# Optimization experiments

Hardware: AMD Instinct MI355X
Metric: run time of the kernel (lower is better)

The kernel has to match this reference:

```python
import jax, jax.numpy as jnp
import numpy as np

B, T, N = 8, 20, 256
BN = B * N
IN_DIM, H, HEADS, DH = 2, 128, 8, 16
FF = 4 * H
LAYERS = 5
EPS = 1e-5


def _ln(h, g, b):
    mu = h.mean(-1, keepdims=True)
    v = ((h - mu) ** 2).mean(-1, keepdims=True)
    return (h - mu) * jax.lax.rsqrt(v + EPS) * g + b


def setup_inputs() -> dict:
    key = jax.random.key(0)
    ks = jax.random.split(key, 16)
    ego_mask = jax.random.uniform(ks[0], (B, T, N)) > 0.2
    ego_mask = ego_mask.at[:, 0, :].set(True)  # every node active at t=0 (no fully-padded sequence)
    x_raw = jax.random.normal(ks[1], (T, BN, IN_DIM), dtype=jnp.float32)
    adj = (jax.random.uniform(ks[2], (T, BN, BN)) < 0.01).astype(jnp.float32)
    s = 0.02
    p = {}
    p['gcn1_w'] = jax.random.normal(ks[3], (IN_DIM, H), jnp.float32) * s
    p['gcn_ws'] = jax.random.normal(ks[4], (5, H, H), jnp.float32) * s
    p['gcn_bs'] = jnp.zeros((6, H), jnp.float32)
    p['ln_g'] = jnp.ones((6, H), jnp.float32)
    p['ln_b'] = jnp.zeros((6, H), jnp.float32)
    p['pos_embed'] = jax.random.normal(ks[5], (T, H), jnp.float32) * s
    p['t_wqkv'] = jax.random.normal(ks[6], (LAYERS, 3 * H, H), jnp.float32) * s
    p['t_bqkv'] = jnp.zeros((LAYERS, 3 * H), jnp.float32)
    p['t_wo'] = jax.random.normal(ks[7], (LAYERS, H, H), jnp.float32) * s
    p['t_bo'] = jnp.zeros((LAYERS, H), jnp.float32)
    p['t_ln1g'] = jnp.ones((LAYERS, H), jnp.float32)
    p['t_ln1b'] = jnp.zeros((LAYERS, H), jnp.float32)
    p['t_w1'] = jax.random.normal(ks[8], (LAYERS, FF, H), jnp.float32) * s
    p['t_b1'] = jnp.zeros((LAYERS, FF), jnp.float32)
    p['t_w2'] = jax.random.normal(ks[9], (LAYERS, H, FF), jnp.float32) * s
    p['t_b2'] = jnp.zeros((LAYERS, H), jnp.float32)
    p['t_ln2g'] = jnp.ones((LAYERS, H), jnp.float32)
    p['t_ln2b'] = jnp.zeros((LAYERS, H), jnp.float32)
    return dict(ego_mask=ego_mask, x_raw=x_raw, adj=adj, **p)


def _forward(ego_mask, x_raw, adj, gcn1_w, gcn_ws, gcn_bs, ln_g, ln_b, pos_embed,
             t_wqkv, t_bqkv, t_wo, t_bo, t_ln1g, t_ln1b, t_w1, t_b1, t_w2, t_b2,
             t_ln2g, t_ln2b):
    mask_flat = ego_mask.transpose(1, 0, 2).reshape(T, BN).astype(x_raw.dtype)  # [T, BN]

    def per_t(x_t, A_t, m):
        # masked subgraph + self-loops only on active nodes (PyG GCNConv on x[idx], A[idx][:,idx])
        Am = A_t * m[:, None] * m[None, :]
        Ahat = Am + jnp.diag(m)
        deg = Ahat.sum(0)                       # gcn_norm: degree at target (col of edge_index)
        dinv = jnp.where(deg > 0, jax.lax.rsqrt(deg), 0.0)
        S = (dinv[:, None] * Ahat * dinv[None, :]).T  # out[dst] = sum_src norm * x[src]

        def gcn(h, W, b):
            return S @ (h @ W) + b

        h = jax.nn.relu(_ln(gcn(x_t, gcn1_w, gcn_bs[0]), ln_g[0], ln_b[0]))
        for i in range(5):
            hr = _ln(gcn(h, gcn_ws[i], gcn_bs[i + 1]), ln_g[i + 1], ln_b[i + 1])
            h = jax.nn.relu(hr + h)  # residual then ReLU, as in source
        return h * m[:, None]        # inactive rows stay zero (x_placeholder)

    x_ph = jax.vmap(per_t)(x_raw, adj, mask_flat)          # [T, BN, H]
    x = x_ph.transpose(1, 0, 2) + pos_embed[None]          # [BN, T, H]

    # src_key_padding_mask: True = padded -> -inf on keys
    key_bias = jnp.where(mask_flat.T.astype(bool), 0.0, -jnp.inf)[:, None, None, :]  # [BN,1,1,T]
    scale = 1.0 / np.sqrt(DH)
    for l in range(LAYERS):  # post-norm TransformerEncoderLayer, activation=relu, eval (no dropout)
        qkv = x @ t_wqkv[l].T + t_bqkv[l]
        q, k, v = jnp.split(qkv, 3, axis=-1)
        q = q.reshape(BN, T, HEADS, DH)
        k = k.reshape(BN, T, HEADS, DH)
        v = v.reshape(BN, T, HEADS, DH)
        sc = jnp.einsum('bqhd,bkhd->bhqk', q, k) * scale + key_bias
        a = jax.nn.softmax(sc, axis=-1)
        o = jnp.einsum('bhqk,bkhd->bqhd', a, v).reshape(BN, T, H)
        o = o @ t_wo[l].T + t_bo[l]
        x = _ln(x + o, t_ln1g[l], t_ln1b[l])
        ff = jax.nn.relu(x @ t_w1[l].T + t_b1[l]) @ t_w2[l].T + t_b2[l]
        x = _ln(x + ff, t_ln2g[l], t_ln2b[l])
    return x.reshape(B, N, T, H)


def reference(ego_mask, x_raw, adj, gcn1_w, gcn_ws, gcn_bs, ln_g, ln_b, pos_embed,
              t_wqkv, t_bqkv, t_wo, t_bo, t_ln1g, t_ln1b, t_w1, t_b1, t_w2, t_b2,
              t_ln2g, t_ln2b):
    return _forward(ego_mask, x_raw, adj, gcn1_w, gcn_ws, gcn_bs, ln_g, ln_b,
                    pos_embed, t_wqkv, t_bqkv, t_wo, t_bo, t_ln1g, t_ln1b,
                    t_w1, t_b1, t_w2, t_b2, t_ln2g, t_ln2b)
```

## Files before the change

kernel.cpp:

```cpp
#include <hip/hip_runtime.h>
#include <hip/hip_bf16.h>
#include <cstdint>
#include <cstddef>

#define BNODES 2048
#define NT 20
#define HDIM 128
#define NROWS (NT * BNODES)
#define CAP 64
#define QP 129

typedef __attribute__((ext_vector_type(8))) short short8;
typedef __attribute__((ext_vector_type(4))) float floatx4;

__device__ __forceinline__ float bf2f(short u) {
  return __uint_as_float(((unsigned int)(unsigned short)u) << 16);
}

__global__ void setup_kernel(const void* __restrict__ ego, float* __restrict__ maskf,
                             int* __restrict__ colcnt,
                             const float* __restrict__ twqkv, const float* __restrict__ two,
                             const float* __restrict__ tw1, const float* __restrict__ tw2,
                             const float* __restrict__ gcnws,
                             __hip_bfloat16* __restrict__ wqkv, __hip_bfloat16* __restrict__ wo,
                             __hip_bfloat16* __restrict__ w1, __hip_bfloat16* __restrict__ w2,
                             __hip_bfloat16* __restrict__ wsT) {
  int gid = blockIdx.x * blockDim.x + threadIdx.x;
  if (gid < NROWS) {
    unsigned int w0 = ((const unsigned int*)ego)[0];
    int val;
    if (w0 == 1u)                 val = ((const int*)ego)[gid] != 0;
    else if (w0 == 0x3F800000u)   val = ((const float*)ego)[gid] != 0.0f;
    else if (w0 == 0x3F803F80u)   val = ((const unsigned short*)ego)[gid] != 0;
    else                          val = ((const unsigned char*)ego)[gid] != 0;
    int b = gid / (NT * 256);
    int t = (gid / 256) % NT;
    int n = gid % 256;
    maskf[t * BNODES + b * 256 + n] = val ? 1.0f : 0.0f;
    colcnt[gid] = 0;
    return;
  }
  gid -= NROWS;
  if (gid < 245760) { wqkv[gid] = __float2bfloat16(twqkv[gid]); return; }
  gid -= 245760;
  if (gid < 81920) { wo[gid] = __float2bfloat16(two[gid]); return; }
  gid -= 81920;
  if (gid < 327680) { w1[gid] = __float2bfloat16(tw1[gid]); return; }
  gid -= 327680;
  if (gid < 327680) { w2[gid] = __float2bfloat16(tw2[gid]); return; }
  gid -= 327680;
  if (gid < 81920) {
    int l = gid >> 14, rem = gid & 16383;
    int n = rem >> 7, k = rem & 127;
    wsT[gid] = __float2bfloat16(gcnws[(l << 14) + (k << 7) + n]);
  }
}

__global__ __launch_bounds__(256) void build_edges_kernel(const float* __restrict__ adj,
                                                          const float* __restrict__ maskf,
                                                          int* __restrict__ colcnt,
                                                          int* __restrict__ colidx) {
  size_t e4 = (size_t)blockIdx.x * 256 + threadIdx.x;
  size_t e = e4 * 4;
  size_t row = e >> 11;
  if (maskf[row] == 0.0f) return;
  const float4 a = ((const float4*)adj)[e4];
  if (a.x == 0.0f && a.y == 0.0f && a.z == 0.0f && a.w == 0.0f) return;
  int i0 = (int)(e & (BNODES - 1));
  int t = (int)(row >> 11);
  int j = (int)(row & (BNODES - 1));
  int base = t * BNODES;
  if (a.x != 0.0f) { int p = atomicAdd(&colcnt[base + i0 + 0], 1); if (p < CAP) colidx[(size_t)(base + i0 + 0) * CAP + p] = j; }
  if (a.y != 0.0f) { int p = atomicAdd(&colcnt[base + i0 + 1], 1); if (p < CAP) colidx[(size_t)(base + i0 + 1) * CAP + p] = j; }
  if (a.z != 0.0f) { int p = atomicAdd(&colcnt[base + i0 + 2], 1); if (p < CAP) colidx[(size_t)(base + i0 + 2) * CAP + p] = j; }
  if (a.w != 0.0f) { int p = atomicAdd(&colcnt[base + i0 + 3], 1); if (p < CAP) colidx[(size_t)(base + i0 + 3) * CAP + p] = j; }
}

__global__ void finalize_deg_kernel(const float* __restrict__ maskf, int* __restrict__ colcnt,
                                    float* __restrict__ dinv) {
  int gid = blockIdx.x * blockDim.x + threadIdx.x;
  if (gid >= NROWS) return;
  int cnt = colcnt[gid];
  dinv[gid] = (maskf[gid] != 0.0f) ? rsqrtf((float)cnt + 1.0f) : 0.0f;
  colcnt[gid] = cnt < CAP ? cnt : CAP;
}

__global__ __launch_bounds__(HDIM) void spmm_ln0_kernel(const float* __restrict__ xraw,
                                                        const float* __restrict__ gw,
                                                        const float* __restrict__ dinv,
                                                        const int* __restrict__ colcnt,
                                                        const int* __restrict__ colidx,
                                                        const float* __restrict__ bias,
                                                        const float* __restrict__ gamma,
                                                        const float* __restrict__ beta,
                                                        float* __restrict__ dstF,
                                                        __hip_bfloat16* __restrict__ dstB) {
  int r = blockIdx.x, c = threadIdx.x;
  int t = r >> 11;
  float di = dinv[r];
  float g0 = gw[c], g1 = gw[HDIM + c];
  float acc = 0.0f;
  if (di != 0.0f) {
    acc = di * fmaf(xraw[2 * r], g0, xraw[2 * r + 1] * g1);
    int cnt = colcnt[r];
    const int* cols = colidx + (size_t)r * CAP;
    const float* dt = dinv + t * BNODES;
    for (int k = 0; k < cnt; ++k) {
      int j = cols[k];
      size_t gr = (size_t)t * BNODES + j;
      acc = fmaf(dt[j], fmaf(xraw[2 * gr], g0, xraw[2 * gr + 1] * g1), acc);
    }
    acc *= di;
  }
  float v = acc + bias[c];
  float s = v, q = v * v;
  #pragma unroll
  for (int off = 32; off > 0; off >>= 1) {
    s += __shfl_down(s, off, 64);
    q += __shfl_down(q, off, 64);
  }
  __shared__ float ls[2], lq2[2];
  int wid = c >> 6, lane = c & 63;
  if (lane == 0) { ls[wid] = s; lq2[wid] = q; }
  __syncthreads();
  float mu = (ls[0] + ls[1]) * (1.0f / HDIM);
  float var = fmaxf((lq2[0] + lq2[1]) * (1.0f / HDIM) - mu * mu, 0.0f);
  float rs = rsqrtf(var + 1e-5f);
  float o = fmaxf((v - mu) * rs * gamma[c] + beta[c], 0.0f);
  size_t oi = (size_t)r * HDIM + c;
  dstF[oi] = o;
  dstB[oi] = __float2bfloat16(o);
}

__global__ __launch_bounds__(HDIM) void spmm_kernel(const __hip_bfloat16* __restrict__ Y,
                                                    const float* __restrict__ dinv,
                                                    const int* __restrict__ colcnt,
                                                    const int* __restrict__ colidx,
                                                    __hip_bfloat16* __restrict__ out) {
  int r = blockIdx.x, c = threadIdx.x;
  int t = r >> 11;
  float di = dinv[r];
  size_t oi = (size_t)r * HDIM + c;
  if (di == 0.0f) { out[oi] = __float2bfloat16(0.0f); return; }
  const short* Ys = (const short*)Y;
  float acc = di * bf2f(Ys[oi]);
  int cnt = colcnt[r];
  const int* cols = colidx + (size_t)r * CAP;
  const float* dt = dinv + t * BNODES;
  const short* Yt = Ys + (size_t)t * BNODES * HDIM;
  for (int k = 0; k < cnt; ++k) {
    int j = cols[k];
    acc = fmaf(dt[j], bf2f(Yt[(size_t)j * HDIM + c]), acc);
  }
  out[oi] = __float2bfloat16(di * acc);
}

__device__ __forceinline__ void async16(const void* g, void* l) {
  __builtin_amdgcn_global_load_lds(
      (const __attribute__((address_space(1))) unsigned int*)g,
      (__attribute__((address_space(3))) unsigned int*)l, 16, 0, 0);
}

__global__ __launch_bounds__(256) void gemm_plain(const __hip_bfloat16* __restrict__ A,
                                                  const __hip_bfloat16* __restrict__ Bt,
                                                  const float* __restrict__ bias,
                                                  int K, int N, int relu,
                                                  __hip_bfloat16* __restrict__ Cb) {
  __shared__ __align__(16) char smem[65536];
  __hip_bfloat16* As = (__hip_bfloat16*)smem;
  __hip_bfloat16* Bs = As + 128 * 128;
  const int tid = threadIdx.x;
  const int wv = tid >> 6, ln = tid & 63;
  const int n0 = blockIdx.x << 7, m0 = blockIdx.y << 7;
  const int wm = (wv & 1) << 6, wn = (wv >> 1) << 6;
  const int lr = ln & 15, lq = ln >> 4;

  floatx4 acc[4][4];
  #pragma unroll
  for (int mi = 0; mi < 4; ++mi)
    #pragma unroll
    for (int ni = 0; ni < 4; ++ni) acc[mi][ni] = (floatx4)0.0f;

  for (int k0 = 0; k0 < K; k0 += 128) {
    if (k0) __syncthreads();
    #pragma unroll
    for (int i = 0; i < 8; ++i) {
      int rloc = i * 16 + wv * 4 + lq;
      int sc = (ln & 15) ^ (rloc & 15);
      async16((const char*)A + ((size_t)(m0 + rloc) * K + k0) * 2 + (size_t)sc * 16,
              (char*)As + (size_t)(i * 16 + wv * 4) * 256);
      async16((const char*)Bt + ((size_t)(n0 + rloc) * K + k0) * 2 + (size_t)sc * 16,
              (char*)Bs + (size_t)(i * 16 + wv * 4) * 256);
    }
    __syncthreads();
    #pragma unroll
    for (int kc = 0; kc < 4; ++kc) {
      short8 af[4], bfr[4];
      #pragma unroll
      for (int mi = 0; mi < 4; ++mi) {
        int R = wm + (mi << 4) + lr;
        int ch = ((kc << 2) + lq) ^ (R & 15);
        af[mi] = *(const short8*)(As + (R << 7) + (ch << 3));
      }
      #pragma unroll
      for (int ni = 0; ni < 4; ++ni) {
        int R = wn + (ni << 4) + lr;
        int ch = ((kc << 2) + lq) ^ (R & 15);
        bfr[ni] = *(const short8*)(Bs + (R << 7) + (ch << 3));
      }
      #pragma unroll
      for (int mi = 0; mi < 4; ++mi)
        #pragma unroll
        for (int ni = 0; ni < 4; ++ni)
          acc[mi][ni] = __builtin_amdgcn_mfma_f32_16x16x32_bf16(af[mi], bfr[ni], acc[mi][ni], 0, 0, 0);
    }
  }
  #pragma unroll
  for (int ni = 0; ni < 4; ++ni) {
    int cn = n0 + wn + (ni << 4) + lr;
    float bv = bias ? bias[cn] : 0.0f;
    #pragma unroll
    for (int mi = 0; mi < 4; ++mi) {
      #pragma unroll
      for (int r = 0; r < 4; ++r) {
        int rm = m0 + wm + (mi << 4) + (lq << 2) + r;
        float v = acc[mi][ni][r] + bv;
        if (relu) v = fmaxf(v, 0.0f);
        Cb[(size_t)rm * N + cn] = __float2bfloat16(v);
      }
    }
  }
}

__global__ __launch_bounds__(256) void gemm_ln(const __hip_bfloat16* __restrict__ A,
                                               const __hip_bfloat16* __restrict__ Bt,
                                               const float* __restrict__ bias,
                                               int K, int gcn_mode,
                                               const float* __restrict__ residF,
                                               const float* __restrict__ lng,
                                               const float* __restrict__ lnb,
                                               const float* __restrict__ maskf,
                                               const float* __restrict__ pos,
                                               float* __restrict__ outF,
                                               __hip_bfloat16* __restrict__ outB) {
  __shared__ __align__(16) char smem[49152];
  __hip_bfloat16* As = (__hip_bfloat16*)smem;
  __hip_bfloat16* Bs = As + 64 * 128;
  float* Cs = (float*)smem;
  const int tid = threadIdx.x;
  const int wv = tid >> 6, ln = tid & 63;
  const int m0 = blockIdx.x << 6;
  const int wm = (wv & 1) << 5, wn = (wv >> 1) << 6;
  const int lr = ln & 15, lq = ln >> 4;

  floatx4 acc[2][4];
  #pragma unroll
  for (int mi = 0; mi < 2; ++mi)
    #pragma unroll
    for (int ni = 0; ni < 4; ++ni) acc[mi][ni] = (floatx4)0.0f;

  for (int k0 = 0; k0 < K; k0 += 128) {
    if (k0) __syncthreads();
    #pragma unroll
    for (int i = 0; i < 4; ++i) {
      int rloc = i * 16 + wv * 4 + lq;
      int sc = (ln & 15) ^ (rloc & 15);
      async16((const char*)A + ((size_t)(m0 + rloc) * K + k0) * 2 + (size_t)sc * 16,
              (char*)As + (size_t)(i * 16 + wv * 4) * 256);
    }
    #pragma unroll
    for (int i = 0; i < 8; ++i) {
      int rloc = i * 16 + wv * 4 + lq;
      int sc = (ln & 15) ^ (rloc & 15);
      async16((const char*)Bt + ((size_t)rloc * K + k0) * 2 + (size_t)sc * 16,
              (char*)Bs + (size_t)(i * 16 + wv * 4) * 256);
    }
    __syncthreads();
    #pragma unroll
    for (int kc = 0; kc < 4; ++kc) {
      short8 af[2], bfr[4];
      #pragma unroll
      for (int mi = 0; mi < 2; ++mi) {
        int R = wm + (mi << 4) + lr;
        int ch = ((kc << 2) + lq) ^ (R & 15);
        af[mi] = *(const short8*)(As + (R << 7) + (ch << 3));
      }
      #pragma unroll
      for (int ni = 0; ni < 4; ++ni) {
        int R = wn + (ni << 4) + lr;
        int ch = ((kc << 2) + lq) ^ (R & 15);
        bfr[ni] = *(const short8*)(Bs + (R << 7) + (ch << 3));
      }
      #pragma unroll
      for (int mi = 0; mi < 2; ++mi)
        #pragma unroll
        for (int ni = 0; ni < 4; ++ni)
          acc[mi][ni] = __builtin_amdgcn_mfma_f32_16x16x32_bf16(af[mi], bfr[ni], acc[mi][ni], 0, 0, 0);
    }
  }

  __syncthreads();
  #pragma unroll
  for (int ni = 0; ni < 4; ++ni) {
    int cn = wn + (ni << 4) + lr;
    float bv = bias[cn];
    #pragma unroll
    for (int mi = 0; mi < 2; ++mi) {
      #pragma unroll
      for (int r = 0; r < 4; ++r) {
        int rl = wm + (mi << 4) + (lq << 2) + r;
        float v = acc[mi][ni][r] + bv;
        if (!gcn_mode) v += residF[(size_t)(m0 + rl) * HDIM + cn];
        Cs[(rl << 7) + cn] = v;
      }
    }
  }
  __syncthreads();
  float2 gam = *(const float2*)(lng + ln * 2);
  float2 bet = *(const float2*)(lnb + ln * 2);
  #pragma unroll 4
  for (int p = 0; p < 16; ++p) {
    int rl = p * 4 + wv;
    int grow = m0 + rl;
    float2 xv = *(const float2*)(Cs + (rl << 7) + ln * 2);
    float s = xv.x + xv.y, q = xv.x * xv.x + xv.y * xv.y;
    #pragma unroll
    for (int off = 32; off > 0; off >>= 1) {
      s += __shfl_xor(s, off, 64);
      q += __shfl_xor(q, off, 64);
    }
    float mu = s * (1.0f / HDIM);
    float var = fmaxf(q * (1.0f / HDIM) - mu * mu, 0.0f);
    float rs = rsqrtf(var + 1e-5f);
    float o0 = (xv.x - mu) * rs * gam.x + bet.x;
    float o1 = (xv.y - mu) * rs * gam.y + bet.y;
    if (gcn_mode) {
      float2 rv = *(const float2*)(residF + (size_t)grow * HDIM + ln * 2);
      o0 = fmaxf(o0 + rv.x, 0.0f);
      o1 = fmaxf(o1 + rv.y, 0.0f);
    }
    size_t oi;
    if (pos) {
      int t = grow >> 11, bn = grow & (BNODES - 1);
      float m = maskf[grow];
      float2 pv = *(const float2*)(pos + t * HDIM + ln * 2);
      o0 = o0 * m + pv.x;
      o1 = o1 * m + pv.y;
      oi = ((size_t)bn * NT + t) * HDIM + ln * 2;
    } else {
      oi = (size_t)grow * HDIM + ln * 2;
    }
    if (outF) *(float2*)(outF + oi) = make_float2(o0, o1);
    if (outB) {
      __hip_bfloat16 b0 = __float2bfloat16(o0), b1 = __float2bfloat16(o1);
      unsigned int pk = ((unsigned int)*(unsigned short*)&b1 << 16) | *(unsigned short*)&b0;
      *(unsigned int*)((char*)outB + oi * 2) = pk;
    }
  }
}

__global__ __launch_bounds__(256) void attn_kernel(const __hip_bfloat16* __restrict__ qkv,
                                                   const float* __restrict__ maskf,
                                                   __hip_bfloat16* __restrict__ o) {
  int bn = blockIdx.x;
  __shared__ float q[NT][QP], kk[NT][QP], vv[NT][QP];
  __shared__ float sc[8][NT][NT];
  __shared__ float mb[NT];
  int tid = threadIdx.x;
  if (tid < NT) mb[tid] = (maskf[tid * BNODES + bn] == 0.0f) ? -1e30f : 0.0f;
  for (int idx = tid; idx < NT * 48; idx += 256) {
    int t = idx / 48, c8 = idx % 48;
    short8 v8 = *(const short8*)((const short*)qkv + ((size_t)bn * NT + t) * 384 + c8 * 8);
    float* dst = (c8 < 16) ? &q[t][c8 * 8] : (c8 < 32) ? &kk[t][(c8 - 16) * 8] : &vv[t][(c8 - 32) * 8];
    #pragma unroll
    for (int i = 0; i < 8; ++i) dst[i] = bf2f(v8[i]);
  }
  __syncthreads();
  for (int idx = tid; idx < 8 * NT * NT; idx += 256) {
    int h = idx / (NT * NT), rr = idx % (NT * NT);
    int tq = rr / NT, tk = rr % NT;
    float s = 0.0f;
    #pragma unroll
    for (int d = 0; d < 16; ++d) s += q[tq][h * 16 + d] * kk[tk][h * 16 + d];
    sc[h][tq][tk] = s * 0.25f + mb[tk];
  }
  __syncthreads();
  if (tid < 8 * NT) {
    int h = tid / NT, tq = tid % NT;
    float mx = -1e30f;
    for (int tk = 0; tk < NT; ++tk) mx = fmaxf(mx, sc[h][tq][tk]);
    float sum = 0.0f;
    for (int tk = 0; tk < NT; ++tk) { float e = __expf(sc[h][tq][tk] - mx); sc[h][tq][tk] = e; sum += e; }
    float inv = 1.0f / sum;
    for (int tk = 0; tk < NT; ++tk) sc[h][tq][tk] *= inv;
  }
  __syncthreads();
  for (int idx = tid; idx < NT * HDIM; idx += 256) {
    int tq = idx / HDIM, col = idx % HDIM;
    int h = col >> 4;
    float s = 0.0f;
    #pragma unroll
    for (int tk = 0; tk < NT; ++tk) s += sc[h][tq][tk] * vv[tk][col];
    o[((size_t)bn * NT + tq) * HDIM + col] = __float2bfloat16(s);
  }
}

extern "C" void kernel_launch(void* const* d_in, const int* in_sizes, int n_in,
                              void* d_out, int out_size, void* d_ws, size_t ws_size,
                              hipStream_t stream) {
  const void*  ego   = d_in[0];
  const float* xraw  = (const float*)d_in[1];
  const float* adj   = (const float*)d_in[2];
  const float* gcn1w = (const float*)d_in[3];
  const float* gcnws = (const float*)d_in[4];
  const float* gcnbs = (const float*)d_in[5];
  const float* lng   = (const float*)d_in[6];
  const float* lnb   = (const float*)d_in[7];
  const float* pos   = (const float*)d_in[8];
  const float* twqkv = (const float*)d_in[9];
  const float* tbqkv = (const float*)d_in[10];
  const float* two   = (const float*)d_in[11];
  const float* tbo   = (const float*)d_in[12];
  const float* tln1g = (const float*)d_in[13];
  const float* tln1b = (const float*)d_in[14];
  const float* tw1   = (const float*)d_in[15];
  const float* tb1   = (const float*)d_in[16];
  const float* tw2   = (const float*)d_in[17];
  const float* tb2   = (const float*)d_in[18];
  const float* tln2g = (const float*)d_in[19];
  const float* tln2b = (const float*)d_in[20];

  char* base = (char*)d_ws;
  size_t off = 0;
  auto alloc = [&](size_t bytes) -> void* {
    void* p = base + off;
    off = (off + bytes + 255) & ~(size_t)255;
    return p;
  };
  float* maskf  = (float*)alloc((size_t)NROWS * 4);
  float* dinv   = (float*)alloc((size_t)NROWS * 4);
  int*   colcnt = (int*)  alloc((size_t)NROWS * 4);
  void*  regA   = alloc((size_t)NROWS * 384 * 2);
  int*   colidx = (int*)regA;
  __hip_bfloat16* qkv_bf = (__hip_bfloat16*)regA;
  void*  regB   = alloc((size_t)NROWS * 512 * 2);
  __hip_bfloat16* g_bf   = (__hip_bfloat16*)regB;
  __hip_bfloat16* big_bf = (__hip_bfloat16*)regB;
  __hip_bfloat16* attn_bf = (__hip_bfloat16*)alloc((size_t)NROWS * HDIM * 2);
  __hip_bfloat16* hbufA   = (__hip_bfloat16*)alloc((size_t)NROWS * HDIM * 2);
  __hip_bfloat16* xbf     = (__hip_bfloat16*)alloc((size_t)NROWS * HDIM * 2);
  float* hbufF  = (float*)alloc((size_t)NROWS * HDIM * 4);
  float* xbuf   = (float*)alloc((size_t)NROWS * HDIM * 4);
  __hip_bfloat16* wqkv_bf = (__hip_bfloat16*)alloc((size_t)245760 * 2);
  __hip_bfloat16* wo_bf   = (__hip_bfloat16*)alloc((size_t)81920 * 2);
  __hip_bfloat16* w1_bf   = (__hip_bfloat16*)alloc((size_t)327680 * 2);
  __hip_bfloat16* w2_bf   = (__hip_bfloat16*)alloc((size_t)327680 * 2);
  __hip_bfloat16* wsT_bf  = (__hip_bfloat16*)alloc((size_t)81920 * 2);

  setup_kernel<<<4320, 256, 0, stream>>>(ego, maskf, colcnt, twqkv, two, tw1, tw2, gcnws,
                                         wqkv_bf, wo_bf, w1_bf, w2_bf, wsT_bf);
  build_edges_kernel<<<81920, 256, 0, stream>>>(adj, maskf, colcnt, colidx);
  finalize_deg_kernel<<<160, 256, 0, stream>>>(maskf, colcnt, dinv);

  spmm_ln0_kernel<<<NROWS, HDIM, 0, stream>>>(xraw, gcn1w, dinv, colcnt, colidx,
                                              gcnbs, lng, lnb, hbufF, hbufA);
  for (int i = 0; i < 5; ++i) {
    spmm_kernel<<<NROWS, HDIM, 0, stream>>>(hbufA, dinv, colcnt, colidx, g_bf);
    const float* fm = (i == 4) ? maskf : nullptr;
    const float* fp = (i == 4) ? pos : nullptr;
    float* oF = (i == 4) ? xbuf : hbufF;
    __hip_bfloat16* oB = (i == 4) ? xbf : hbufA;
    gemm_ln<<<NROWS / 64, 256, 0, stream>>>(
        g_bf, wsT_bf + (size_t)i * 16384, gcnbs + (i + 1) * 128, 128, 1,
        hbufF, lng + (i + 1) * 128, lnb + (i + 1) * 128, fm, fp, oF, oB);
  }

  for (int l = 0; l < 5; ++l) {
    gemm_plain<<<dim3(3, NROWS / 128), 256, 0, stream>>>(
        xbf, wqkv_bf + (size_t)l * 49152, tbqkv + l * 384, 128, 384, 0, qkv_bf);
    attn_kernel<<<BNODES, 256, 0, stream>>>(qkv_bf, maskf, attn_bf);
    gemm_ln<<<NROWS / 64, 256, 0, stream>>>(
        attn_bf, wo_bf + (size_t)l * 16384, tbo + l * 128, 128, 0,
        xbuf, tln1g + l * 128, tln1b + l * 128, nullptr, nullptr, xbuf, xbf);
    gemm_plain<<<dim3(4, NROWS / 128), 256, 0, stream>>>(
        xbf, w1_bf + (size_t)l * 65536, tb1 + l * 512, 128, 512, 1, big_bf);
    float* oF = (l == 4) ? (float*)d_out : xbuf;
    __hip_bfloat16* oB = (l == 4) ? nullptr : xbf;
    gemm_ln<<<NROWS / 64, 256, 0, stream>>>(
        big_bf, w2_bf + (size_t)l * 65536, tb2 + l * 128, 512, 0,
        xbuf, tln2g + l * 128, tln2b + l * 128, nullptr, nullptr, oF, oB);
  }
}
```

Baseline: 1.530 ms.

## Use one wavefront per row in SpMM kernels and fuse attention per thread

The SpMM and first-layer GCN kernels now map one 64-lane wavefront to each row, with two columns per lane. They load and store packed bf16 pairs and do the layer-norm reduction with xor shuffles instead of shared memory and a block barrier. The attention kernel drops the shared score matrix and its two extra barriers: each of the 160 threads handles one (head, query) pair, keeps scores and outputs in registers, and writes 16 bf16 values as vector stores. In exchange, the attention kernel uses more registers per thread and leaves about 96 of its 256 threads idle after the load phase.

```diff
diff --git a/kernel.cpp b/kernel.cpp
--- a/kernel.cpp
+++ b/kernel.cpp
@@ -15,6 +15,10 @@
 
 __device__ __forceinline__ float bf2f(short u) {
   return __uint_as_float(((unsigned int)(unsigned short)u) << 16);
+}
+__device__ __forceinline__ unsigned int pack2(float a, float b) {
+  __hip_bfloat16 b0 = __float2bfloat16(a), b1 = __float2bfloat16(b);
+  return ((unsigned int)*(unsigned short*)&b1 << 16) | *(unsigned short*)&b0;
 }
 
 __global__ void setup_kernel(const void* __restrict__ ego, float* __restrict__ maskf,
@@ -85,74 +89,87 @@
   colcnt[gid] = cnt < CAP ? cnt : CAP;
 }
 
-__global__ __launch_bounds__(HDIM) void spmm_ln0_kernel(const float* __restrict__ xraw,
-                                                        const float* __restrict__ gw,
-                                                        const float* __restrict__ dinv,
-                                                        const int* __restrict__ colcnt,
-                                                        const int* __restrict__ colidx,
-                                                        const float* __restrict__ bias,
-                                                        const float* __restrict__ gamma,
-                                                        const float* __restrict__ beta,
-                                                        float* __restrict__ dstF,
-                                                        __hip_bfloat16* __restrict__ dstB) {
-  int r = blockIdx.x, c = threadIdx.x;
+__global__ __launch_bounds__(256) void spmm_ln0_kernel(const float* __restrict__ xraw,
+                                                       const float* __restrict__ gw,
+                                                       const float* __restrict__ dinv,
+                                                       const int* __restrict__ colcnt,
+                                                       const int* __restrict__ colidx,
+                                                       const float* __restrict__ bias,
+                                                       const float* __restrict__ gamma,
+                                                       const float* __restrict__ beta,
+                                                       float* __restrict__ dstF,
+                                                       __hip_bfloat16* __restrict__ dstB) {
+  int tid = threadIdx.x;
+  int r = (blockIdx.x << 2) + (tid >> 6);
+  int lane = tid & 63;
+  int c0 = lane << 1;
   int t = r >> 11;
   float di = dinv[r];
-  float g0 = gw[c], g1 = gw[HDIM + c];
-  float acc = 0.0f;
+  float g00 = gw[c0], g01 = gw[c0 + 1], g10 = gw[HDIM + c0], g11 = gw[HDIM + c0 + 1];
+  float a0 = 0.0f, a1 = 0.0f;
   if (di != 0.0f) {
-    acc = di * fmaf(xraw[2 * r], g0, xraw[2 * r + 1] * g1);
+    float x0 = xraw[2 * r], x1 = xraw[2 * r + 1];
+    a0 = di * fmaf(x0, g00, x1 * g10);
+    a1 = di * fmaf(x0, g01, x1 * g11);
     int cnt = colcnt[r];
     const int* cols = colidx + (size_t)r * CAP;
-    const float* dt = dinv + t * BNODES;
+    const float* dt = dinv + (t << 11);
     for (int k = 0; k < cnt; ++k) {
       int j = cols[k];
-      size_t gr = (size_t)t * BNODES + j;
-      acc = fmaf(dt[j], fmaf(xraw[2 * gr], g0, xraw[2 * gr + 1] * g1), acc);
-    }
-    acc *= di;
-  }
-  float v = acc + bias[c];
-  float s = v, q = v * v;
+      size_t gr = ((size_t)t << 11) + j;
+      float y0 = xraw[2 * gr], y1 = xraw[2 * gr + 1];
+      float dj = dt[j];
+      a0 = fmaf(dj, fmaf(y0, g00, y1 * g10), a0);
+      a1 = fmaf(dj, fmaf(y0, g01, y1 * g11), a1);
+    }
+    a0 *= di; a1 *= di;
+  }
+  a0 += bias[c0]; a1 += bias[c0 + 1];
+  float s = a0 + a1, q = a0 * a0 + a1 * a1;
   #pragma unroll
   for (int off = 32; off > 0; off >>= 1) {
-    s += __shfl_down(s, off, 64);
-    q += __shfl_down(q, off, 64);
-  }
-  __shared__ float ls[2], lq2[2];
-  int wid = c >> 6, lane = c & 63;
-  if (lane == 0) { ls[wid] = s; lq2[wid] = q; }
-  __syncthreads();
-  float mu = (ls[0] + ls[1]) * (1.0f / HDIM);
-  float var = fmaxf((lq2[0] + lq2[1]) * (1.0f / HDIM) - mu * mu, 0.0f);
+    s += __shfl_xor(s, off, 64);
+    q += __shfl_xor(q, off, 64);
+  }
+  float mu = s * (1.0f / HDIM);
+  float var = fmaxf(q * (1.0f / HDIM) - mu * mu, 0.0f);
   float rs = rsqrtf(var + 1e-5f);
-  float o = fmaxf((v - mu) * rs * gamma[c] + beta[c], 0.0f);
-  size_t oi = (size_t)r * HDIM + c;
-  dstF[oi] = o;
-  dstB[oi] = __float2bfloat16(o);
-}
-
-__global__ __launch_bounds__(HDIM) void spmm_kernel(const __hip_bfloat16* __restrict__ Y,
-                                                    const float* __restrict__ dinv,
-                                                    const int* __restrict__ colcnt,
-                                                    const int* __restrict__ colidx,
-                                                    __hip_bfloat16* __restrict__ out) {
-  int r = blockIdx.x, c = threadIdx.x;
+  float o0 = fmaxf((a0 - mu) * rs * gamma[c0] + beta[c0], 0.0f);
+  float o1 = fmaxf((a1 - mu) * rs * gamma[c0 + 1] + beta[c0 + 1], 0.0f);
+  size_t oi = (size_t)r * HDIM + c0;
+  *(float2*)(dstF + oi) = make_float2(o0, o1);
+  *(unsigned int*)((char*)dstB + oi * 2) = pack2(o0, o1);
+}
+
+__global__ __launch_bounds__(256) void spmm_kernel(const __hip_bfloat16* __restrict__ Y,
+                                                   const float* __restrict__ dinv,
+                                                   const int* __restrict__ colcnt,
+                                                   const int* __restrict__ colidx,
+                                                   __hip_bfloat16* __restrict__ out) {
+  int tid = threadIdx.x;
+  int r = (blockIdx.x << 2) + (tid >> 6);
+  int lane = tid & 63;
   int t = r >> 11;
   float di = dinv[r];
-  size_t oi = (size_t)r * HDIM + c;
-  if (di == 0.0f) { out[oi] = __float2bfloat16(0.0f); return; }
-  const short* Ys = (const short*)Y;
-  float acc = di * bf2f(Ys[oi]);
+  const unsigned int* Yrow = (const unsigned int*)((const short*)Y + (size_t)r * HDIM) + lane;
+  unsigned int* orow = (unsigned int*)((short*)out + (size_t)r * HDIM) + lane;
+  if (di == 0.0f) { *orow = 0u; return; }
+  unsigned int sv = *Yrow;
+  float a0 = di * bf2f((short)(sv & 0xffff));
+  float a1 = di * bf2f((short)(sv >> 16));
   int cnt = colcnt[r];
   const int* cols = colidx + (size_t)r * CAP;
-  const float* dt = dinv + t * BNODES;
-  const short* Yt = Ys + (size_t)t * BNODES * HDIM;
+  const float* dt = dinv + (t << 11);
+  const unsigned int* Yt = (const unsigned int*)((const short*)Y + (((size_t)t << 11) * HDIM)) + lane;
   for (int k = 0; k < cnt; ++k) {
     int j = cols[k];
-    acc = fmaf(dt[j], bf2f(Yt[(size_t)j * HDIM + c]), acc);
-  }
-  out[oi] = __float2bfloat16(di * acc);
+    float dj = dt[j];
+    unsigned int v = Yt[(size_t)j << 6];
+    a0 = fmaf(dj, bf2f((short)(v & 0xffff)), a0);
+    a1 = fmaf(dj, bf2f((short)(v >> 16)), a1);
+  }
+  a0 *= di; a1 *= di;
+  *orow = pack2(a0, a1);
 }
 
 __device__ __forceinline__ void async16(const void* g, void* l) {
@@ -351,11 +368,7 @@
       oi = (size_t)grow * HDIM + ln * 2;
     }
     if (outF) *(float2*)(outF + oi) = make_float2(o0, o1);
-    if (outB) {
-      __hip_bfloat16 b0 = __float2bfloat16(o0), b1 = __float2bfloat16(o1);
-      unsigned int pk = ((unsigned int)*(unsigned short*)&b1 << 16) | *(unsigned short*)&b0;
-      *(unsigned int*)((char*)outB + oi * 2) = pk;
-    }
+    if (outB) *(unsigned int*)((char*)outB + oi * 2) = pack2(o0, o1);
   }
 }
 
@@ -364,7 +377,6 @@
                                                    __hip_bfloat16* __restrict__ o) {
   int bn = blockIdx.x;
   __shared__ float q[NT][QP], kk[NT][QP], vv[NT][QP];
-  __shared__ float sc[8][NT][NT];
   __shared__ float mb[NT];
   int tid = threadIdx.x;
   if (tid < NT) mb[tid] = (maskf[tid * BNODES + bn] == 0.0f) ? -1e30f : 0.0f;
@@ -376,33 +388,49 @@
     for (int i = 0; i < 8; ++i) dst[i] = bf2f(v8[i]);
   }
   __syncthreads();
-  for (int idx = tid; idx < 8 * NT * NT; idx += 256) {
-    int h = idx / (NT * NT), rr = idx % (NT * NT);
-    int tq = rr / NT, tk = rr % NT;
+  if (tid >= 8 * NT) return;
+  int h = tid / NT, tq = tid % NT;
+  float qr[16];
+  #pragma unroll
+  for (int d = 0; d < 16; ++d) qr[d] = q[tq][h * 16 + d];
+  float p[NT];
+  float mx = -1e30f;
+  #pragma unroll
+  for (int tk = 0; tk < NT; ++tk) {
     float s = 0.0f;
     #pragma unroll
-    for (int d = 0; d < 16; ++d) s += q[tq][h * 16 + d] * kk[tk][h * 16 + d];
-    sc[h][tq][tk] = s * 0.25f + mb[tk];
-  }
-  __syncthreads();
-  if (tid < 8 * NT) {
-    int h = tid / NT, tq = tid % NT;
-    float mx = -1e30f;
-    for (int tk = 0; tk < NT; ++tk) mx = fmaxf(mx, sc[h][tq][tk]);
-    float sum = 0.0f;
-    for (int tk = 0; tk < NT; ++tk) { float e = __expf(sc[h][tq][tk] - mx); sc[h][tq][tk] = e; sum += e; }
-    float inv = 1.0f / sum;
-    for (int tk = 0; tk < NT; ++tk) sc[h][tq][tk] *= inv;
-  }
-  __syncthreads();
-  for (int idx = tid; idx < NT * HDIM; idx += 256) {
-    int tq = idx / HDIM, col = idx % HDIM;
-    int h = col >> 4;
-    float s = 0.0f;
-    #pragma unroll
-    for (int tk = 0; tk < NT; ++tk) s += sc[h][tq][tk] * vv[tk][col];
-    o[((size_t)bn * NT + tq) * HDIM + col] = __float2bfloat16(s);
-  }
+    for (int d = 0; d < 16; ++d) s = fmaf(qr[d], kk[tk][h * 16 + d], s);
+    s = s * 0.25f + mb[tk];
+    p[tk] = s;
+    mx = fmaxf(mx, s);
+  }
+  float sum = 0.0f;
+  #pragma unroll
+  for (int tk = 0; tk < NT; ++tk) { float e = __expf(p[tk] - mx); p[tk] = e; sum += e; }
+  float inv = 1.0f / sum;
+  float oacc[16];
+  #pragma unroll
+  for (int d = 0; d < 16; ++d) oacc[d] = 0.0f;
+  #pragma unroll
+  for (int tk = 0; tk < NT; ++tk) {
+    float pv = p[tk] * inv;
+    #pragma unroll
+    for (int d = 0; d < 16; ++d) oacc[d] = fmaf(pv, vv[tk][h * 16 + d], oacc[d]);
+  }
+  short* op = (short*)o + ((size_t)bn * NT + tq) * HDIM + h * 16;
+  short8 o8a, o8b;
+  #pragma unroll
+  for (int d = 0; d < 8; ++d) {
+    __hip_bfloat16 b = __float2bfloat16(oacc[d]);
+    o8a[d] = *(short*)&b;
+  }
+  #pragma unroll
+  for (int d = 0; d < 8; ++d) {
+    __hip_bfloat16 b = __float2bfloat16(oacc[8 + d]);
+    o8b[d] = *(short*)&b;
+  }
+  *(short8*)op = o8a;
+  *(short8*)(op + 8) = o8b;
 }
 
 extern "C" void kernel_launch(void* const* d_in, const int* in_sizes, int n_in,
@@ -462,10 +490,10 @@
   build_edges_kernel<<<81920, 256, 0, stream>>>(adj, maskf, colcnt, colidx);
   finalize_deg_kernel<<<160, 256, 0, stream>>>(maskf, colcnt, dinv);
 
-  spmm_ln0_kernel<<<NROWS, HDIM, 0, stream>>>(xraw, gcn1w, dinv, colcnt, colidx,
-                                              gcnbs, lng, lnb, hbufF, hbufA);
+  spmm_ln0_kernel<<<NROWS / 4, 256, 0, stream>>>(xraw, gcn1w, dinv, colcnt, colidx,
+                                                 gcnbs, lng, lnb, hbufF, hbufA);
   for (int i = 0; i < 5; ++i) {
-    spmm_kernel<<<NROWS, HDIM, 0, stream>>>(hbufA, dinv, colcnt, colidx, g_bf);
+    spmm_kernel<<<NROWS / 4, 256, 0, stream>>>(hbufA, dinv, colcnt, colidx, g_bf);
     const float* fm = (i == 4) ? maskf : nullptr;
     const float* fp = (i == 4) ? pos : nullptr;
     float* oF = (i == 4) ? xbuf : hbufF;
```

Measured after the change: 1.495 ms. 2.2% less time.
